# Kernel optimization log

Hardware: AMD Instinct MI355X
Metric: run time of the kernel (lower is better)

Reference implementation:

```python
import jax, jax.numpy as jnp
import numpy as np

WS = 49        # window size
NH = 8         # num heads


def setup_inputs() -> dict:
    key = jax.random.key(0)
    k1, k2, k3 = jax.random.split(key, 3)
    B, N, C = 4, 50176, 512
    x = jax.random.normal(k1, (B, N, C), dtype=jnp.float32)
    w_qkv = jax.random.normal(k2, (3 * C, C), dtype=jnp.float32) * (C ** -0.5)
    b_qkv = jnp.zeros((3 * C,), dtype=jnp.float32)
    w_proj = jax.random.normal(k3, (C, C), dtype=jnp.float32) * (C ** -0.5)
    b_proj = jnp.zeros((C,), dtype=jnp.float32)
    return {"x": x, "w_qkv": w_qkv, "b_qkv": b_qkv, "w_proj": w_proj, "b_proj": b_proj}


def reference(x, w_qkv, b_qkv, w_proj, b_proj):
    B, N, C = x.shape
    w = N // WS
    hd = C // NH
    scale = hd ** -0.5
    # shuffle: 'b (ws w) c -> (b w) ws c'  (outer factor is ws -> strided windows)
    xw = x.reshape(B, WS, w, C).transpose(0, 2, 1, 3).reshape(B * w, WS, C)
    qkv = xw @ w_qkv.T + b_qkv                       # [(B w), WS, 3C]
    qkv = qkv.reshape(B * w, WS, 3, NH, hd)
    q = qkv[:, :, 0].transpose(0, 2, 1, 3) * scale   # [(B w), NH, WS, hd]
    k = qkv[:, :, 1].transpose(0, 2, 1, 3)
    v = qkv[:, :, 2].transpose(0, 2, 1, 3)
    attn = jax.nn.softmax(jnp.einsum('bhqd,bhkd->bhqk', q, k), axis=-1)
    out = jnp.einsum('bhqk,bhkd->bhqd', attn, v)     # [(B w), NH, WS, hd]
    out = out.transpose(0, 2, 1, 3).reshape(B * w, WS, C)
    out = out @ w_proj.T + b_proj
    # unshuffle: '(b w) ws c -> b (ws w) c'
    out = out.reshape(B, w, WS, C).transpose(0, 2, 1, 3).reshape(B, N, C)
    return out
```

## Files before the change

### kernel.cpp

```cpp
#include <hip/hip_runtime.h>
#include <cstdint>
#include <cstddef>


typedef __bf16 bf16x8 __attribute__((ext_vector_type(8)));
typedef __bf16 bf16x4 __attribute__((ext_vector_type(4)));
typedef float  f32x4  __attribute__((ext_vector_type(4)));

#define MFMA_BF16(a, b, c) __builtin_amdgcn_mfma_f32_16x16x32_bf16((a), (b), (c), 0, 0, 0)

static __device__ __forceinline__ int swzi(int row, int col) {
  return col ^ ((row & 7) << 3);
}
static __device__ __forceinline__ int gswz(int row, int col) {
  return col ^ (((row >> 1) & 3) << 3);
}

typedef __attribute__((address_space(1))) const void gconst_t;
typedef __attribute__((address_space(3))) void lds_t;
static __device__ __forceinline__ void gload16(const void* g, void* l) {
  __builtin_amdgcn_global_load_lds((gconst_t*)g, (lds_t*)l, 16, 0, 0);
}

static __device__ __forceinline__ int wm2tok(int m) {
  const int b   = m / 50176;
  const int rem = m - b * 50176;
  const int wi  = rem / 49;
  const int s   = rem - wi * 49;
  return b * 50176 + s * 1024 + wi;
}

__global__ void prep_weights(const float* __restrict__ wqkv,
                             const float* __restrict__ bqkv,
                             const float* __restrict__ wproj,
                             __bf16* __restrict__ wqkv_bf,
                             __bf16* __restrict__ wproj_bf,
                             float* __restrict__ bq_s) {
  const int stride = gridDim.x * blockDim.x;
  const int t0 = blockIdx.x * blockDim.x + threadIdx.x;
  for (int i = t0; i < 1536 * 512; i += stride) {
    float v = wqkv[i];
    if (i < 512 * 512) v *= 0.125f;
    wqkv_bf[i] = (__bf16)v;
  }
  for (int i = t0; i < 512 * 512; i += stride) wproj_bf[i] = (__bf16)wproj[i];
  for (int i = t0; i < 1536; i += stride)      bq_s[i] = (i < 512 ? 0.125f : 1.0f) * bqkv[i];
}

__global__ void prep_x(const float* __restrict__ x, __bf16* __restrict__ xb) {
  const size_t total  = (size_t)200704 * 64;
  const size_t stride = (size_t)gridDim.x * blockDim.x;
  for (size_t i = (size_t)blockIdx.x * blockDim.x + threadIdx.x; i < total; i += stride) {
    const int m  = (int)(i >> 6);
    const int c8 = ((int)i & 63) * 8;
    const size_t t = (size_t)wm2tok(m);
    const float4 a = *(const float4*)(x + t * 512 + c8);
    const float4 b = *(const float4*)(x + t * 512 + c8 + 4);
    bf16x8 v;
    v[0] = (__bf16)a.x; v[1] = (__bf16)a.y; v[2] = (__bf16)a.z; v[3] = (__bf16)a.w;
    v[4] = (__bf16)b.x; v[5] = (__bf16)b.y; v[6] = (__bf16)b.z; v[7] = (__bf16)b.w;
    *(bf16x8*)(xb + i * 8) = v;
  }
}

template<bool OUT_F32, bool PERM_OUT>
__launch_bounds__(256)
__global__ void gemm_bt(const __bf16* __restrict__ Ab,
                        const __bf16* __restrict__ Bw,
                        const float* __restrict__ bias,
                        void* __restrict__ Cv,
                        int Mtiles, int Ntiles) {
  __shared__ __align__(16) __bf16 sA[2][128 * 32];
  __shared__ __align__(16) __bf16 sB[2][128 * 32];

  const int tid  = threadIdx.x;
  const int lane = tid & 63;
  const int l15  = lane & 15;
  const int kg   = ((lane >> 4) & 3) * 8;
  const int r4   = ((lane >> 4) & 3) * 4;
  const int wv   = tid >> 6, wm = wv >> 1, wn = wv & 1;

  const int nwg = Mtiles * Ntiles;
  const int cpx = nwg >> 3;
  const int wg  = (blockIdx.x & 7) * cpx + (blockIdx.x >> 3);
  const int mt  = wg / Ntiles;
  const int nt  = wg % Ntiles;
  const size_t m0 = (size_t)mt * 128;
  const int    n0 = nt * 128;

  const int srow  = tid >> 2;
  const int scol8 = ((tid & 3) * 8) ^ (((tid >> 3) & 3) << 3);

  f32x4 acc[4][4];
  const f32x4 zf = {0.f, 0.f, 0.f, 0.f};
#pragma unroll
  for (int i = 0; i < 4; ++i)
#pragma unroll
    for (int j = 0; j < 4; ++j) acc[i][j] = zf;

#pragma unroll
  for (int j = 0; j < 2; ++j) {
    gload16(Bw + ((size_t)(n0 + j * 64 + srow)) * 512 + scol8,
            &sB[0][0] + (size_t)tid * 8 + j * 2048);
    gload16(Ab + (m0 + j * 64 + srow) * 512 + scol8,
            &sA[0][0] + (size_t)tid * 8 + j * 2048);
  }
  __syncthreads();

  int buf = 0;
  for (int kt = 0; kt < 16; ++kt) {
    const int k1 = (kt + 1) * 32;
    if (kt < 15) {
#pragma unroll
      for (int j = 0; j < 2; ++j) {
        gload16(Bw + ((size_t)(n0 + j * 64 + srow)) * 512 + k1 + scol8,
                &sB[buf ^ 1][0] + (size_t)tid * 8 + j * 2048);
        gload16(Ab + (m0 + j * 64 + srow) * 512 + k1 + scol8,
                &sA[buf ^ 1][0] + (size_t)tid * 8 + j * 2048);
      }
    }
    bf16x8 af[4], bfr[4];
#pragma unroll
    for (int m = 0; m < 4; ++m) {
      const int row = wm * 64 + m * 16 + l15;
      af[m] = *(const bf16x8*)&sA[buf][row * 32 + gswz(row, kg)];
    }
#pragma unroll
    for (int n = 0; n < 4; ++n) {
      const int row = wn * 64 + n * 16 + l15;
      bfr[n] = *(const bf16x8*)&sB[buf][row * 32 + gswz(row, kg)];
    }
#pragma unroll
    for (int m = 0; m < 4; ++m)
#pragma unroll
      for (int n = 0; n < 4; ++n)
        acc[m][n] = MFMA_BF16(af[m], bfr[n], acc[m][n]);

    __syncthreads();
    buf ^= 1;
  }

  const int Nld = Ntiles * 128;
#pragma unroll
  for (int m = 0; m < 4; ++m) {
#pragma unroll
    for (int r = 0; r < 4; ++r) {
      const int row = (int)m0 + wm * 64 + m * 16 + r4 + r;
      const size_t orow = PERM_OUT ? (size_t)wm2tok(row) : (size_t)row;
#pragma unroll
      for (int n = 0; n < 4; ++n) {
        const int col = n0 + wn * 64 + n * 16 + l15;
        const float v = acc[m][n][r] + bias[col];
        if (OUT_F32) ((float*)Cv)[orow * (size_t)Nld + col] = v;
        else         ((__bf16*)Cv)[orow * (size_t)Nld + col] = (__bf16)v;
      }
    }
  }
}

__launch_bounds__(512)
__global__ void attn_win(const __bf16* __restrict__ qkv, __bf16* __restrict__ O) {
  __shared__ __align__(16) __bf16 vT[8 * 64 * 64];
  __shared__ __align__(16) __bf16 sP[8][16 * 64];

  const int tid  = threadIdx.x;
  const int lane = tid & 63;
  const int h    = tid >> 6;
  const int l15  = lane & 15;
  const int kg   = ((lane >> 4) & 3) * 8;
  const int r4   = ((lane >> 4) & 3) * 4;

  const size_t wbase = (size_t)blockIdx.x * 49;

  const int MOFF[4] = {0, 16, 32, 33};
  const float NEG_INF = -__builtin_inff();

  bf16x8 aq[4][2], bk[4][2];
#pragma unroll
  for (int mt = 0; mt < 4; ++mt) {
    const size_t tok = wbase + (size_t)(MOFF[mt] + l15);
#pragma unroll
    for (int ks = 0; ks < 2; ++ks) {
      aq[mt][ks] = *(const bf16x8*)(qkv + tok * 1536 +       h * 64 + ks * 32 + kg);
      bk[mt][ks] = *(const bf16x8*)(qkv + tok * 1536 + 512 + h * 64 + ks * 32 + kg);
    }
  }

  for (int i = tid; i < 8 * 64 * 16; i += 512) {
    const int k = 48 + (i & 15);
    if (k != 48) {
      const int n  = (i >> 4) & 63;
      const int hh = i >> 10;
      vT[hh * 4096 + n * 64 + (k ^ ((n & 7) << 3))] = (__bf16)0.0f;
    }
  }
  for (int i = tid; i < 49 * 64; i += 512) {
    const int s  = i >> 6;
    const int c8 = (i & 63) * 8;
    bf16x8 v8 = *(const bf16x8*)(qkv + (wbase + s) * 1536 + 1024 + c8);
    const int hh = c8 >> 6;
#pragma unroll
    for (int j = 0; j < 8; ++j) {
      const int n = (c8 & 63) + j;
      vT[hh * 4096 + n * 64 + (s ^ ((n & 7) << 3))] = v8[j];
    }
  }
  __syncthreads();

  bf16x8 bv[4][2];
#pragma unroll
  for (int ntv = 0; ntv < 4; ++ntv) {
    const int n = ntv * 16 + l15;
#pragma unroll
    for (int ks = 0; ks < 2; ++ks)
      bv[ntv][ks] = *(const bf16x8*)&vT[h * 4096 + n * 64 + ((ks * 32 + kg) ^ ((n & 7) << 3))];
  }

  f32x4 accS[4][4];
  const f32x4 zf = {0.f, 0.f, 0.f, 0.f};
#pragma unroll
  for (int m = 0; m < 4; ++m)
#pragma unroll
    for (int n = 0; n < 4; ++n) accS[m][n] = zf;
#pragma unroll
  for (int ks = 0; ks < 2; ++ks)
#pragma unroll
    for (int m = 0; m < 4; ++m)
#pragma unroll
      for (int n = 0; n < 4; ++n)
        accS[m][n] = MFMA_BF16(aq[m][ks], bk[n][ks], accS[m][n]);

#pragma unroll
  for (int mt = 0; mt < 4; ++mt) {
#pragma unroll
    for (int r = 0; r < 4; ++r) {
      const int prow = r4 + r;
      const float sv0 = accS[mt][0][r];
      const float sv1 = accS[mt][1][r];
      const float sv2 = accS[mt][2][r];
      const float sv3 = (l15 == 15) ? accS[mt][3][r] : NEG_INF;
      float mx = fmaxf(fmaxf(sv0, sv1), fmaxf(sv2, sv3));
      mx = fmaxf(mx, __shfl_xor(mx, 1));
      mx = fmaxf(mx, __shfl_xor(mx, 2));
      mx = fmaxf(mx, __shfl_xor(mx, 4));
      mx = fmaxf(mx, __shfl_xor(mx, 8));
      const float e0 = __expf(sv0 - mx);
      const float e1 = __expf(sv1 - mx);
      const float e2 = __expf(sv2 - mx);
      const float e3 = __expf(sv3 - mx);
      float sum = e0 + e1 + e2 + e3;
      sum += __shfl_xor(sum, 1);
      sum += __shfl_xor(sum, 2);
      sum += __shfl_xor(sum, 4);
      sum += __shfl_xor(sum, 8);
      const float inv = 1.0f / sum;
      sP[h][prow * 64 + swzi(prow, 0  + l15)] = (__bf16)(e0 * inv);
      sP[h][prow * 64 + swzi(prow, 16 + l15)] = (__bf16)(e1 * inv);
      sP[h][prow * 64 + swzi(prow, 32 + l15)] = (__bf16)(e2 * inv);
      if (l15 == 15) sP[h][prow * 64 + swzi(prow, 48)] = (__bf16)(e3 * inv);
      if (l15 < 15)  sP[h][prow * 64 + swzi(prow, 49 + l15)] = (__bf16)0.0f;
    }
    bf16x8 ap[2];
#pragma unroll
    for (int ks = 0; ks < 2; ++ks)
      ap[ks] = *(const bf16x8*)&sP[h][l15 * 64 + swzi(l15, ks * 32 + kg)];
    f32x4 accO[4];
#pragma unroll
    for (int n = 0; n < 4; ++n) accO[n] = zf;
#pragma unroll
    for (int ks = 0; ks < 2; ++ks)
#pragma unroll
      for (int n = 0; n < 4; ++n)
        accO[n] = MFMA_BF16(ap[ks], bv[n][ks], accO[n]);
#pragma unroll
    for (int n = 0; n < 4; ++n) {
#pragma unroll
      for (int r = 0; r < 4; ++r) {
        const int row = MOFF[mt] + r4 + r;
        O[(wbase + row) * 512 + h * 64 + n * 16 + l15] = (__bf16)accO[n][r];
      }
    }
  }
}

__launch_bounds__(256, 2)
__global__ void swin_attn_fused(const float* __restrict__ x,
                                const __bf16* __restrict__ wqkv_bf,
                                const float* __restrict__ bq_s,
                                const __bf16* __restrict__ wproj_bf,
                                const float* __restrict__ bproj,
                                float* __restrict__ out) {
  __shared__ __align__(16) __bf16 s_xw[49 * 512];
  __shared__ __align__(16) __bf16 s_q [49 * 64];
  __shared__ __align__(16) __bf16 s_k [49 * 64];
  __shared__ __align__(16) __bf16 s_vT[64 * 64];
  __shared__ __align__(16) __bf16 s_p [49 * 64];

  const int tid  = threadIdx.x;
  const int lane = tid & 63;
  const int wv   = tid >> 6;
  const int l15  = lane & 15;
  const int kg   = (lane >> 4) * 8;
  const int r4   = (lane >> 4) * 4;
  const int blk = blockIdx.x;
  const int b   = blk >> 10;
  const int wi  = blk & 1023;
  const int MOFF[4] = {0, 16, 32, 33};
  const float NEG_INF = -__builtin_inff();

  for (int i = tid; i < 64 * 64; i += 256) s_vT[i] = (__bf16)0.0f;
  const float* xwin = x + ((size_t)b * 50176 + (size_t)wi) * 512;
  for (int idx = tid; idx < 49 * 128; idx += 256) {
    const int row = idx >> 7;
    const int c4  = (idx & 127) * 4;
    const float4 v = *(const float4*)(xwin + (size_t)row * (1024 * 512) + c4);
    bf16x4 t;
    t.x = (__bf16)v.x; t.y = (__bf16)v.y; t.z = (__bf16)v.z; t.w = (__bf16)v.w;
    *(bf16x4*)&s_xw[row * 512 + swzi(row, c4)] = t;
  }
  f32x4 accF[4][8];
  const f32x4 zf = {0.f, 0.f, 0.f, 0.f};
#pragma unroll
  for (int m = 0; m < 4; ++m)
#pragma unroll
    for (int n = 0; n < 8; ++n) accF[m][n] = zf;
  __syncthreads();

  for (int h = 0; h < 8; ++h) {
    f32x4 accA[4][3];
#pragma unroll
    for (int m = 0; m < 4; ++m)
#pragma unroll
      for (int n = 0; n < 3; ++n) accA[m][n] = zf;
    const __bf16* pB[3];
    float biasv[3];
#pragma unroll
    for (int nt = 0; nt < 3; ++nt) {
      const int c  = wv * 48 + nt * 16 + l15;
      const int wr = (c < 64) ? (h * 64 + c)
                   : (c < 128) ? (512 + h * 64 + (c - 64))
                               : (1024 + h * 64 + (c - 128));
      pB[nt]    = wqkv_bf + (size_t)wr * 512 + kg;
      biasv[nt] = bq_s[wr];
    }
#pragma unroll
    for (int ks = 0; ks < 16; ++ks) {
      bf16x8 a[4], bb[3];
#pragma unroll
      for (int mt = 0; mt < 4; ++mt) {
        const int row = MOFF[mt] + l15;
        a[mt] = *(const bf16x8*)&s_xw[row * 512 + swzi(row, ks * 32 + kg)];
      }
#pragma unroll
      for (int nt = 0; nt < 3; ++nt) bb[nt] = *(const bf16x8*)(pB[nt] + ks * 32);
#pragma unroll
      for (int mt = 0; mt < 4; ++mt)
#pragma unroll
        for (int nt = 0; nt < 3; ++nt)
          accA[mt][nt] = MFMA_BF16(a[mt], bb[nt], accA[mt][nt]);
    }
#pragma unroll
    for (int nt = 0; nt < 3; ++nt) {
      const int c = wv * 48 + nt * 16 + l15;
#pragma unroll
      for (int mt = 0; mt < 4; ++mt) {
#pragma unroll
        for (int r = 0; r < 4; ++r) {
          const int row = MOFF[mt] + r4 + r;
          const __bf16 bvv = (__bf16)(accA[mt][nt][r] + biasv[nt]);
          if (c < 64)       s_q[row * 64 + swzi(row, c)] = bvv;
          else if (c < 128) s_k[row * 64 + swzi(row, c - 64)] = bvv;
          else {
            const int vr = c - 128;
            s_vT[vr * 64 + swzi(vr, row)] = bvv;
          }
        }
      }
    }
    __syncthreads();

    const int R = MOFF[wv];
    bf16x8 aq[2], bkf[4][2];
#pragma unroll
    for (int ks2 = 0; ks2 < 2; ++ks2) {
      const int row = R + l15;
      aq[ks2] = *(const bf16x8*)&s_q[row * 64 + swzi(row, ks2 * 32 + kg)];
    }
#pragma unroll
    for (int nt = 0; nt < 4; ++nt) {
      const int row = MOFF[nt] + l15;
#pragma unroll
      for (int ks2 = 0; ks2 < 2; ++ks2)
        bkf[nt][ks2] = *(const bf16x8*)&s_k[row * 64 + swzi(row, ks2 * 32 + kg)];
    }
    f32x4 accS[4];
#pragma unroll
    for (int n = 0; n < 4; ++n) accS[n] = zf;
#pragma unroll
    for (int ks2 = 0; ks2 < 2; ++ks2)
#pragma unroll
      for (int nt = 0; nt < 4; ++nt)
        accS[nt] = MFMA_BF16(aq[ks2], bkf[nt][ks2], accS[nt]);
#pragma unroll
    for (int r = 0; r < 4; ++r) {
      const int row = R + r4 + r;
      const float sv0 = accS[0][r];
      const float sv1 = accS[1][r];
      const float sv2 = accS[2][r];
      const float sv3 = (l15 == 15) ? accS[3][r] : NEG_INF;
      float m = fmaxf(fmaxf(sv0, sv1), fmaxf(sv2, sv3));
      m = fmaxf(m, __shfl_xor(m, 1));
      m = fmaxf(m, __shfl_xor(m, 2));
      m = fmaxf(m, __shfl_xor(m, 4));
      m = fmaxf(m, __shfl_xor(m, 8));
      const float e0 = __expf(sv0 - m);
      const float e1 = __expf(sv1 - m);
      const float e2 = __expf(sv2 - m);
      const float e3 = __expf(sv3 - m);
      float s = e0 + e1 + e2 + e3;
      s += __shfl_xor(s, 1);
      s += __shfl_xor(s, 2);
      s += __shfl_xor(s, 4);
      s += __shfl_xor(s, 8);
      const float inv = 1.0f / s;
      s_p[row * 64 + swzi(row, 0  + l15)] = (__bf16)(e0 * inv);
      s_p[row * 64 + swzi(row, 16 + l15)] = (__bf16)(e1 * inv);
      s_p[row * 64 + swzi(row, 32 + l15)] = (__bf16)(e2 * inv);
      if (l15 == 15) s_p[row * 64 + swzi(row, 48)] = (__bf16)(e3 * inv);
      if (l15 < 15)  s_p[row * 64 + swzi(row, 49 + l15)] = (__bf16)0.0f;
    }
    bf16x8 ap[2], bv2[4][2];
#pragma unroll
    for (int ks2 = 0; ks2 < 2; ++ks2) {
      const int row = R + l15;
      ap[ks2] = *(const bf16x8*)&s_p[row * 64 + swzi(row, ks2 * 32 + kg)];
    }
#pragma unroll
    for (int nt = 0; nt < 4; ++nt) {
      const int row = nt * 16 + l15;
#pragma unroll
      for (int ks2 = 0; ks2 < 2; ++ks2)
        bv2[nt][ks2] = *(const bf16x8*)&s_vT[row * 64 + swzi(row, ks2 * 32 + kg)];
    }
    __syncthreads();
    f32x4 accO[4];
#pragma unroll
    for (int n = 0; n < 4; ++n) accO[n] = zf;
#pragma unroll
    for (int ks2 = 0; ks2 < 2; ++ks2)
#pragma unroll
      for (int nt = 0; nt < 4; ++nt)
        accO[nt] = MFMA_BF16(ap[ks2], bv2[nt][ks2], accO[nt]);
#pragma unroll
    for (int nt = 0; nt < 4; ++nt) {
#pragma unroll
      for (int r = 0; r < 4; ++r) {
        const int row = R + r4 + r;
        s_p[row * 64 + swzi(row, nt * 16 + l15)] = (__bf16)accO[nt][r];
      }
    }
    __syncthreads();
#pragma unroll
    for (int ks2 = 0; ks2 < 2; ++ks2) {
      bf16x8 ao[4], bw[8];
#pragma unroll
      for (int mt = 0; mt < 4; ++mt) {
        const int row = MOFF[mt] + l15;
        ao[mt] = *(const bf16x8*)&s_p[row * 64 + swzi(row, ks2 * 32 + kg)];
      }
#pragma unroll
      for (int nt = 0; nt < 8; ++nt) {
        const int cc = wv * 128 + nt * 16 + l15;
        bw[nt] = *(const bf16x8*)(wproj_bf + (size_t)cc * 512 + h * 64 + ks2 * 32 + kg);
      }
#pragma unroll
      for (int mt = 0; mt < 4; ++mt)
#pragma unroll
        for (int nt = 0; nt < 8; ++nt)
          accF[mt][nt] = MFMA_BF16(ao[mt], bw[nt], accF[mt][nt]);
    }
  }
#pragma unroll
  for (int nt = 0; nt < 8; ++nt) {
    const int cc = wv * 128 + nt * 16 + l15;
    const float bp = bproj[cc];
#pragma unroll
    for (int mt = 0; mt < 4; ++mt) {
#pragma unroll
      for (int r = 0; r < 4; ++r) {
        const int row = MOFF[mt] + r4 + r;
        if (mt < 3 || (r4 + r) == 15) {
          out[((size_t)b * 50176 + (size_t)row * 1024 + (size_t)wi) * 512 + cc] =
              accF[mt][nt][r] + bp;
        }
      }
    }
  }
}

extern "C" void kernel_launch(void* const* d_in, const int* in_sizes, int n_in,
                              void* d_out, int out_size, void* d_ws, size_t ws_size,
                              hipStream_t stream) {
  const float* x      = (const float*)d_in[0];
  const float* w_qkv  = (const float*)d_in[1];
  const float* b_qkv  = (const float*)d_in[2];
  const float* w_proj = (const float*)d_in[3];
  const float* b_proj = (const float*)d_in[4];
  float* outp = (float*)d_out;

  const size_t QKV_E = (size_t)200704 * 1536;
  const size_t O_E   = (size_t)200704 * 512;
  const size_t NEED  = (QKV_E + O_E + 786432 + 262144) * 2 + 1536 * 4;

  if (ws_size >= NEED) {
    __bf16* qkv      = (__bf16*)d_ws;
    __bf16* Obuf     = qkv + QKV_E;
    __bf16* wqkv_bf  = Obuf + O_E;
    __bf16* wproj_bf = wqkv_bf + 786432;
    float*  bq_s     = (float*)(wproj_bf + 262144);

    prep_weights<<<512, 256, 0, stream>>>(w_qkv, b_qkv, w_proj, wqkv_bf, wproj_bf, bq_s);
    prep_x<<<2048, 256, 0, stream>>>(x, Obuf);
    gemm_bt<false, false><<<1568 * 12, 256, 0, stream>>>(Obuf, wqkv_bf, bq_s, qkv, 1568, 12);
    attn_win<<<4096, 512, 0, stream>>>(qkv, Obuf);
    gemm_bt<true, true><<<1568 * 4, 256, 0, stream>>>(Obuf, wproj_bf, b_proj, outp, 1568, 4);
  } else {
    __bf16* wqkv_bf  = (__bf16*)d_ws;
    __bf16* wproj_bf = wqkv_bf + 1536 * 512;
    float*  bq_s     = (float*)(wproj_bf + 512 * 512);
    prep_weights<<<1024, 256, 0, stream>>>(w_qkv, b_qkv, w_proj, wqkv_bf, wproj_bf, bq_s);
    swin_attn_fused<<<4096, 256, 0, stream>>>(x, wqkv_bf, bq_s, wproj_bf, b_proj, outp);
  }
}
```

Before: 1.163 ms.

## Enlarge GEMM tiles to 256x256x64 with 8 waves and interleaved async staging

Replaces the 128x128x32 bf16 GEMM with a 256x256 tile, K-step 64, and 512 threads (8 waves, each computing 128x64). Global-to-LDS loads for the next stage are split into halves and interleaved between MFMA groups, using explicit vmcnt waits, raw barriers and setprio so copy and compute overlap. An XOR swizzle on 16-byte chunks replaces the old swizzle. The larger tile raises arithmetic intensity and cuts redundant operand loads, but uses 128 KB of LDS and many more accumulator registers, which limits occupancy; the hand-counted vmcnt waits also make correctness depend on exact load ordering.

```diff
diff --git a/kernel.cpp b/kernel.cpp
--- a/kernel.cpp
+++ b/kernel.cpp
@@ -11,9 +11,6 @@
 
 static __device__ __forceinline__ int swzi(int row, int col) {
   return col ^ ((row & 7) << 3);
-}
-static __device__ __forceinline__ int gswz(int row, int col) {
-  return col ^ (((row >> 1) & 3) << 3);
 }
 
 typedef __attribute__((address_space(1))) const void gconst_t;
@@ -21,6 +18,9 @@
 static __device__ __forceinline__ void gload16(const void* g, void* l) {
   __builtin_amdgcn_global_load_lds((gconst_t*)g, (lds_t*)l, 16, 0, 0);
 }
+
+#define WAITV2()   asm volatile("s_waitcnt vmcnt(2)" ::: "memory")
+#define WAITV0()   asm volatile("s_waitcnt vmcnt(0)" ::: "memory")
 
 static __device__ __forceinline__ int wm2tok(int m) {
   const int b   = m / 50176;
@@ -64,88 +64,113 @@
 }
 
 template<bool OUT_F32, bool PERM_OUT>
-__launch_bounds__(256)
-__global__ void gemm_bt(const __bf16* __restrict__ Ab,
+__launch_bounds__(512, 2)
+__global__ void gemm256(const __bf16* __restrict__ Ab,
                         const __bf16* __restrict__ Bw,
                         const float* __restrict__ bias,
                         void* __restrict__ Cv,
                         int Mtiles, int Ntiles) {
-  __shared__ __align__(16) __bf16 sA[2][128 * 32];
-  __shared__ __align__(16) __bf16 sB[2][128 * 32];
+  __shared__ __align__(16) __bf16 sA[2][256 * 64];
+  __shared__ __align__(16) __bf16 sB[2][256 * 64];
 
   const int tid  = threadIdx.x;
   const int lane = tid & 63;
   const int l15  = lane & 15;
-  const int kg   = ((lane >> 4) & 3) * 8;
-  const int r4   = ((lane >> 4) & 3) * 4;
-  const int wv   = tid >> 6, wm = wv >> 1, wn = wv & 1;
+  const int kgc  = (lane >> 4) & 3;
+  const int r4   = kgc * 4;
+  const int wv   = tid >> 6;
+  const int wm   = wv >> 2, wn = wv & 3;
 
   const int nwg = Mtiles * Ntiles;
   const int cpx = nwg >> 3;
   const int wg  = (blockIdx.x & 7) * cpx + (blockIdx.x >> 3);
   const int mt  = wg / Ntiles;
   const int nt  = wg % Ntiles;
-  const size_t m0 = (size_t)mt * 128;
-  const int    n0 = nt * 128;
-
-  const int srow  = tid >> 2;
-  const int scol8 = ((tid & 3) * 8) ^ (((tid >> 3) & 3) << 3);
-
-  f32x4 acc[4][4];
+  const size_t m0 = (size_t)mt * 256;
+  const int    n0 = nt * 256;
+
+  const int srow   = tid >> 3;
+  const int schunk = (tid & 7) ^ (srow & 7);
+
+  f32x4 acc[8][4];
   const f32x4 zf = {0.f, 0.f, 0.f, 0.f};
 #pragma unroll
-  for (int i = 0; i < 4; ++i)
+  for (int i = 0; i < 8; ++i)
 #pragma unroll
     for (int j = 0; j < 4; ++j) acc[i][j] = zf;
 
-#pragma unroll
-  for (int j = 0; j < 2; ++j) {
-    gload16(Bw + ((size_t)(n0 + j * 64 + srow)) * 512 + scol8,
-            &sB[0][0] + (size_t)tid * 8 + j * 2048);
-    gload16(Ab + (m0 + j * 64 + srow) * 512 + scol8,
-            &sA[0][0] + (size_t)tid * 8 + j * 2048);
-  }
-  __syncthreads();
+  auto STAGE_HALF = [&](int bufi, int kt, int mat, int h) {
+    const size_t kof = (size_t)kt * 64 + schunk * 8;
+    const __bf16* src = mat ? Bw : Ab;
+    const size_t base0 = mat ? (size_t)n0 : m0;
+    __bf16* dst = (mat ? &sB[bufi][0] : &sA[bufi][0]) + h * 8192 + tid * 8;
+#pragma unroll
+    for (int j = 0; j < 2; ++j)
+      gload16(src + (base0 + (size_t)(h * 128 + j * 64 + srow)) * 512 + kof,
+              dst + j * 4096);
+  };
+
+  auto LDB = [&](int bufi, int ks, bf16x8* bfrag) {
+#pragma unroll
+    for (int n = 0; n < 4; ++n) {
+      const int r = wn * 64 + n * 16 + l15;
+      bfrag[n] = *(const bf16x8*)&sB[bufi][r * 64 + (((ks * 4 + kgc) ^ (r & 7)) * 8)];
+    }
+  };
+  auto LDA = [&](int bufi, int mh, int ks, bf16x8* afrag) {
+#pragma unroll
+    for (int m2 = 0; m2 < 4; ++m2) {
+      const int r = wm * 128 + mh * 64 + m2 * 16 + l15;
+      afrag[m2] = *(const bf16x8*)&sA[bufi][r * 64 + (((ks * 4 + kgc) ^ (r & 7)) * 8)];
+    }
+  };
+  auto MM = [&](int mh, const bf16x8* afrag, const bf16x8* bfrag) {
+    __builtin_amdgcn_s_setprio(1);
+#pragma unroll
+    for (int m2 = 0; m2 < 4; ++m2)
+#pragma unroll
+      for (int n = 0; n < 4; ++n)
+        acc[mh * 4 + m2][n] = MFMA_BF16(afrag[m2], bfrag[n], acc[mh * 4 + m2][n]);
+    __builtin_amdgcn_s_setprio(0);
+  };
+
+  STAGE_HALF(0, 0, 0, 0); STAGE_HALF(0, 0, 0, 1);
+  STAGE_HALF(0, 0, 1, 0); STAGE_HALF(0, 0, 1, 1);
 
   int buf = 0;
-  for (int kt = 0; kt < 16; ++kt) {
-    const int k1 = (kt + 1) * 32;
-    if (kt < 15) {
-#pragma unroll
-      for (int j = 0; j < 2; ++j) {
-        gload16(Bw + ((size_t)(n0 + j * 64 + srow)) * 512 + k1 + scol8,
-                &sB[buf ^ 1][0] + (size_t)tid * 8 + j * 2048);
-        gload16(Ab + (m0 + j * 64 + srow) * 512 + k1 + scol8,
-                &sA[buf ^ 1][0] + (size_t)tid * 8 + j * 2048);
-      }
-    }
-    bf16x8 af[4], bfr[4];
-#pragma unroll
-    for (int m = 0; m < 4; ++m) {
-      const int row = wm * 64 + m * 16 + l15;
-      af[m] = *(const bf16x8*)&sA[buf][row * 32 + gswz(row, kg)];
-    }
-#pragma unroll
-    for (int n = 0; n < 4; ++n) {
-      const int row = wn * 64 + n * 16 + l15;
-      bfr[n] = *(const bf16x8*)&sB[buf][row * 32 + gswz(row, kg)];
-    }
-#pragma unroll
-    for (int m = 0; m < 4; ++m)
-#pragma unroll
-      for (int n = 0; n < 4; ++n)
-        acc[m][n] = MFMA_BF16(af[m], bfr[n], acc[m][n]);
-
-    __syncthreads();
-    buf ^= 1;
-  }
-
-  const int Nld = Ntiles * 128;
-#pragma unroll
-  for (int m = 0; m < 4; ++m) {
+  for (int t = 0; t < 8; ++t) {
+    const int nxt = buf ^ 1;
+    if (t < 7) { STAGE_HALF(nxt, t + 1, 0, 0); WAITV2(); }
+    else       { WAITV0(); }
+    __builtin_amdgcn_s_barrier();
+    __builtin_amdgcn_sched_barrier(0);
+
+    bf16x8 b0[4], b1[4], a[4];
+    LDB(buf, 0, b0);
+    LDA(buf, 0, 0, a);
+    MM(0, a, b0);
+    if (t < 7) STAGE_HALF(nxt, t + 1, 0, 1);
+    LDA(buf, 1, 0, a);
+    MM(1, a, b0);
+    if (t < 7) STAGE_HALF(nxt, t + 1, 1, 0);
+    LDB(buf, 1, b1);
+    LDA(buf, 0, 1, a);
+    MM(0, a, b1);
+    if (t < 7) STAGE_HALF(nxt, t + 1, 1, 1);
+    LDA(buf, 1, 1, a);
+    MM(1, a, b1);
+
+    __builtin_amdgcn_sched_barrier(0);
+    __builtin_amdgcn_s_barrier();
+    buf = nxt;
+  }
+
+  const int Nld = Ntiles * 256;
+#pragma unroll
+  for (int m = 0; m < 8; ++m) {
 #pragma unroll
     for (int r = 0; r < 4; ++r) {
-      const int row = (int)m0 + wm * 64 + m * 16 + r4 + r;
+      const int row = (int)m0 + wm * 128 + m * 16 + r4 + r;
       const size_t orow = PERM_OUT ? (size_t)wm2tok(row) : (size_t)row;
 #pragma unroll
       for (int n = 0; n < 4; ++n) {
@@ -521,9 +546,9 @@
 
     prep_weights<<<512, 256, 0, stream>>>(w_qkv, b_qkv, w_proj, wqkv_bf, wproj_bf, bq_s);
     prep_x<<<2048, 256, 0, stream>>>(x, Obuf);
-    gemm_bt<false, false><<<1568 * 12, 256, 0, stream>>>(Obuf, wqkv_bf, bq_s, qkv, 1568, 12);
+    gemm256<false, false><<<784 * 6, 512, 0, stream>>>(Obuf, wqkv_bf, bq_s, qkv, 784, 6);
     attn_win<<<4096, 512, 0, stream>>>(qkv, Obuf);
-    gemm_bt<true, true><<<1568 * 4, 256, 0, stream>>>(Obuf, wproj_bf, b_proj, outp, 1568, 4);
+    gemm256<true, true><<<784 * 2, 512, 0, stream>>>(Obuf, wproj_bf, b_proj, outp, 784, 2);
   } else {
     __bf16* wqkv_bf  = (__bf16*)d_ws;
     __bf16* wproj_bf = wqkv_bf + 1536 * 512;
```

New measurement: 1.067 ms. 8.3% less time.
